# Performance work log

Measured on AMD Instinct MI355X. Metric: run time of the kernel, lower is better.

Reference implementation:

```python
import jax, jax.numpy as jnp
import numpy as np

USER_NUM = 100000
ITEM_NUM = 50000
N_NODES = USER_NUM + ITEM_NUM
EMB_DIM = 64
N_LAYERS = 3
NNZ = 4800000


def setup_inputs() -> dict:
    key = jax.random.key(0)
    k1, k2, k3, k4, k5 = jax.random.split(key, 5)
    user_emb = 0.2 * jax.random.normal(k1, (USER_NUM, EMB_DIM), dtype=jnp.float32)
    item_emb = 0.2 * jax.random.normal(k2, (ITEM_NUM, EMB_DIM), dtype=jnp.float32)
    adj_row = jax.random.randint(k3, (NNZ,), 0, N_NODES, dtype=jnp.int32)
    adj_col = jax.random.randint(k4, (NNZ,), 0, N_NODES, dtype=jnp.int32)
    adj_vals = jax.random.uniform(k5, (NNZ,), dtype=jnp.float32)
    return {
        "user_emb": user_emb,
        "item_emb": item_emb,
        "adj_row": adj_row,
        "adj_col": adj_col,
        "adj_vals": adj_vals,
    }


def _spmm(row, col, vals, x):
    # sparse [N,N] @ dense [N,D] via gather + weighted segment-sum
    msg = vals[:, None] * x[col]  # [nnz, D]
    return jax.ops.segment_sum(msg, row, num_segments=N_NODES)


def reference(user_emb, item_emb, adj_row, adj_col, adj_vals):
    ego = jnp.concatenate([user_emb, item_emb], axis=0)  # [N, D]
    acc = ego  # running sum over layers (equivalent to stack+mean)
    for _ in range(N_LAYERS):
        ego = _spmm(adj_row, adj_col, adj_vals, ego)
        acc = acc + ego
    out = acc / jnp.asarray(N_LAYERS + 1, dtype=acc.dtype)
    return out[:USER_NUM], out[USER_NUM:]
```

## Files before the change

kernel.cpp:

```cpp
#include <hip/hip_runtime.h>

#define USER_NUM 100000
#define ITEM_NUM 50000
#define N_NODES  150000
#define EMB_DIM  64
#define NNZ      4800000

#define CB_SHIFT 10
#define ROWS_PER_CB 1024
#define NCB ((N_NODES + ROWS_PER_CB - 1) / ROWS_PER_CB)
#define CB_CAP 34000
#define TILE 8192
#define NTILES ((NNZ + TILE - 1) / TILE)
#define EPT 32

#define SCAN_ITEMS 1024
#define NUM_SCAN_BLOCKS ((N_NODES + SCAN_ITEMS - 1) / SCAN_ITEMS)

__device__ __forceinline__ float bflo(unsigned u) {
    return __uint_as_float(u << 16);
}
__device__ __forceinline__ float bfhi(unsigned u) {
    return __uint_as_float(u & 0xFFFF0000u);
}
__device__ __forceinline__ unsigned f2bf(float f) {
    unsigned u = __float_as_uint(f);
    return (u + 0x7FFFu + ((u >> 16) & 1u)) >> 16;
}

__global__ void lgcn_init(const float4* __restrict__ user,
                          const float4* __restrict__ item,
                          uint4* __restrict__ xb,
                          float4* __restrict__ acc) {
    int i = blockIdx.x * blockDim.x + threadIdx.x;
    if (i >= N_NODES * 8) return;
    const int user_chunks = USER_NUM * 8;
    float4 f0, f1;
    if (i < user_chunks) {
        f0 = user[i * 2];
        f1 = user[i * 2 + 1];
    } else {
        f0 = item[(i - user_chunks) * 2];
        f1 = item[(i - user_chunks) * 2 + 1];
    }
    acc[i * 2]     = f0;
    acc[i * 2 + 1] = f1;
    uint4 p;
    p.x = f2bf(f0.x) | (f2bf(f0.y) << 16);
    p.y = f2bf(f0.z) | (f2bf(f0.w) << 16);
    p.z = f2bf(f1.x) | (f2bf(f1.y) << 16);
    p.w = f2bf(f1.z) | (f2bf(f1.w) << 16);
    xb[i] = p;
}

__global__ void lgcn_bcur_init(int* __restrict__ bucket_cursor) {
    int b = blockIdx.x * blockDim.x + threadIdx.x;
    if (b < NCB) bucket_cursor[b] = b * CB_CAP;
}

__global__ __launch_bounds__(256) void lgcn_partition(
    const int* __restrict__ row,
    const int* __restrict__ col,
    const float* __restrict__ vals,
    int* __restrict__ bucket_cursor,
    int2* __restrict__ t_cv) {
    __shared__ int hist[NCB];
    __shared__ int excl[NCB];
    __shared__ int delta[NCB];
    __shared__ unsigned lslot[TILE];
    __shared__ int sscan[256];

    int tid = threadIdx.x;
    int tileStart = blockIdx.x * TILE;
    int tileCount = NNZ - tileStart;
    if (tileCount > TILE) tileCount = TILE;

    for (int b = tid; b < NCB; b += 256) hist[b] = 0;
    __syncthreads();

    int rws[EPT];
#pragma unroll
    for (int k = 0; k < EPT; ++k) {
        int le = tid + k * 256;
        int r = -1;
        if (le < tileCount) {
            r = row[tileStart + le];
            atomicAdd(&hist[r >> CB_SHIFT], 1);
        }
        rws[k] = r;
    }
    __syncthreads();

    int h = (tid < NCB) ? hist[tid] : 0;
    sscan[tid] = h;
    __syncthreads();
    for (int off = 1; off < 256; off <<= 1) {
        int x = (tid >= off) ? sscan[tid - off] : 0;
        __syncthreads();
        sscan[tid] += x;
        __syncthreads();
    }
    if (tid < NCB) {
        int ex = sscan[tid] - h;
        excl[tid] = ex;
        int rb = h ? atomicAdd(&bucket_cursor[tid], h) : 0;
        delta[tid] = rb - ex;
    }
    __syncthreads();

#pragma unroll
    for (int k = 0; k < EPT; ++k) {
        int le = tid + k * 256;
        if (le < tileCount) {
            int r = rws[k];
            int b = r >> CB_SHIFT;
            int lp = atomicAdd(&excl[b], 1);
            lslot[lp] = ((unsigned)b << 23) |
                        ((unsigned)(r & (ROWS_PER_CB - 1)) << 13) |
                        (unsigned)le;
        }
    }
    __syncthreads();

    for (int i = tid; i < tileCount; i += 256) {
        unsigned s = lslot[i];
        int b = s >> 23;
        int rlo = (s >> 13) & (ROWS_PER_CB - 1);
        int le = s & 8191;
        int e = tileStart + le;
        int gpos = delta[b] + i;
        if (gpos < (b + 1) * CB_CAP) {
            t_cv[gpos] = make_int2((rlo << 18) | col[e],
                                   __float_as_int(vals[e]));
        }
    }
}

__global__ __launch_bounds__(256) void lgcn_count(
    const int* __restrict__ bucket_cursor,
    const int2* __restrict__ t_cv,
    int* __restrict__ cnt) {
    __shared__ int hist[ROWS_PER_CB];
    int b = blockIdx.x;
    int lo = b * ROWS_PER_CB;
    int nrows = N_NODES - lo;
    if (nrows > ROWS_PER_CB) nrows = ROWS_PER_CB;
    for (int i = threadIdx.x; i < nrows; i += 256) hist[i] = 0;
    __syncthreads();
    int base = b * CB_CAP;
    int count = bucket_cursor[b] - base;
    if (count > CB_CAP) count = CB_CAP;
    for (int e = base + threadIdx.x; e < base + count; e += 256) {
        unsigned rc = (unsigned)t_cv[e].x;
        atomicAdd(&hist[rc >> 18], 1);
    }
    __syncthreads();
    for (int i = threadIdx.x; i < nrows; i += 256) cnt[lo + i] = hist[i];
}

__global__ void lgcn_scan_blocksums(const int* __restrict__ cnt,
                                    int* __restrict__ blockSum) {
    int b = blockIdx.x, t = threadIdx.x;
    int base = b * SCAN_ITEMS + t * 4;
    int s = 0;
#pragma unroll
    for (int k = 0; k < 4; ++k) {
        int i = base + k;
        if (i < N_NODES) s += cnt[i];
    }
    __shared__ int red[256];
    red[t] = s;
    __syncthreads();
    for (int off = 128; off > 0; off >>= 1) {
        if (t < off) red[t] += red[t + off];
        __syncthreads();
    }
    if (t == 0) blockSum[b] = red[0];
}

__global__ void lgcn_scan_sums(const int* __restrict__ blockSum,
                               int* __restrict__ blockBase,
                               int* __restrict__ row_ptr) {
    int t = threadIdx.x;
    __shared__ int s[256];
    int v = (t < NUM_SCAN_BLOCKS) ? blockSum[t] : 0;
    s[t] = v;
    __syncthreads();
    for (int off = 1; off < 256; off <<= 1) {
        int x = (t >= off) ? s[t - off] : 0;
        __syncthreads();
        s[t] += x;
        __syncthreads();
    }
    if (t < NUM_SCAN_BLOCKS) blockBase[t] = s[t] - v;
    if (t == 0) row_ptr[N_NODES] = NNZ;
}

__global__ void lgcn_scan_final(const int* __restrict__ cnt,
                                const int* __restrict__ blockBase,
                                int* __restrict__ row_ptr) {
    int b = blockIdx.x, t = threadIdx.x;
    int base = b * SCAN_ITEMS + t * 4;
    int v[4];
    int tsum = 0;
#pragma unroll
    for (int k = 0; k < 4; ++k) {
        int i = base + k;
        v[k] = (i < N_NODES) ? cnt[i] : 0;
        tsum += v[k];
    }
    __shared__ int s[256];
    s[t] = tsum;
    __syncthreads();
    for (int off = 1; off < 256; off <<= 1) {
        int x = (t >= off) ? s[t - off] : 0;
        __syncthreads();
        s[t] += x;
        __syncthreads();
    }
    int p = blockBase[b] + (s[t] - tsum);
#pragma unroll
    for (int k = 0; k < 4; ++k) {
        int i = base + k;
        if (i < N_NODES) row_ptr[i] = p;
        p += v[k];
    }
}

__global__ __launch_bounds__(256) void lgcn_bucket_scatter(
    const int* __restrict__ row_ptr,
    const int* __restrict__ bucket_cursor,
    const int2* __restrict__ t_cv,
    int2* __restrict__ csr_cv) {
    __shared__ int cur[ROWS_PER_CB];
    int b = blockIdx.x;
    int lo = b * ROWS_PER_CB;
    int nrows = N_NODES - lo;
    if (nrows > ROWS_PER_CB) nrows = ROWS_PER_CB;
    for (int i = threadIdx.x; i < nrows; i += 256)
        cur[i] = row_ptr[lo + i];
    __syncthreads();
    int base = b * CB_CAP;
    int count = bucket_cursor[b] - base;
    if (count > CB_CAP) count = CB_CAP;
    for (int e = base + threadIdx.x; e < base + count; e += 256) {
        int2 cv = t_cv[e];
        int rlo = (unsigned)cv.x >> 18;
        int pos = atomicAdd(&cur[rlo], 1);
        csr_cv[pos] = make_int2(cv.x & 0x3FFFF, cv.y);
    }
}

__global__ __launch_bounds__(256) void lgcn_spmm_bf16(
    const int* __restrict__ row_ptr,
    const int2* __restrict__ csr_cv,
    const uint4* __restrict__ xb,
    uint4* __restrict__ yb,
    float4* __restrict__ acc,
    float scale) {
    int gid = blockIdx.x * blockDim.x + threadIdx.x;
    int r = gid >> 6;
    if (r >= N_NODES) return;
    int lane = threadIdx.x & 63;
    int c = lane & 7;
    int sub = lane >> 3;

    int start = row_ptr[r];
    int end = row_ptr[r + 1];

    float a0[8] = {0.f, 0.f, 0.f, 0.f, 0.f, 0.f, 0.f, 0.f};
    float a1[8] = {0.f, 0.f, 0.f, 0.f, 0.f, 0.f, 0.f, 0.f};

    int e = start + sub;
    for (; e + 8 < end; e += 16) {
        int2 cv0 = csr_cv[e];
        int2 cv1 = csr_cv[e + 8];
        uint4 u0 = xb[cv0.x * 8 + c];
        uint4 u1 = xb[cv1.x * 8 + c];
        float v0 = __int_as_float(cv0.y);
        float v1 = __int_as_float(cv1.y);
        a0[0] += v0 * bflo(u0.x); a0[1] += v0 * bfhi(u0.x);
        a0[2] += v0 * bflo(u0.y); a0[3] += v0 * bfhi(u0.y);
        a0[4] += v0 * bflo(u0.z); a0[5] += v0 * bfhi(u0.z);
        a0[6] += v0 * bflo(u0.w); a0[7] += v0 * bfhi(u0.w);
        a1[0] += v1 * bflo(u1.x); a1[1] += v1 * bfhi(u1.x);
        a1[2] += v1 * bflo(u1.y); a1[3] += v1 * bfhi(u1.y);
        a1[4] += v1 * bflo(u1.z); a1[5] += v1 * bfhi(u1.z);
        a1[6] += v1 * bflo(u1.w); a1[7] += v1 * bfhi(u1.w);
    }
    if (e < end) {
        int2 cv = csr_cv[e];
        uint4 u = xb[cv.x * 8 + c];
        float v = __int_as_float(cv.y);
        a0[0] += v * bflo(u.x); a0[1] += v * bfhi(u.x);
        a0[2] += v * bflo(u.y); a0[3] += v * bfhi(u.y);
        a0[4] += v * bflo(u.z); a0[5] += v * bfhi(u.z);
        a0[6] += v * bflo(u.w); a0[7] += v * bfhi(u.w);
    }

    float a[8];
#pragma unroll
    for (int k = 0; k < 8; ++k) a[k] = a0[k] + a1[k];

#pragma unroll
    for (int k = 0; k < 8; ++k) {
        a[k] += __shfl_xor(a[k], 8);
        a[k] += __shfl_xor(a[k], 16);
        a[k] += __shfl_xor(a[k], 32);
    }

    if (sub == 0) {
        uint4 p;
        p.x = f2bf(a[0]) | (f2bf(a[1]) << 16);
        p.y = f2bf(a[2]) | (f2bf(a[3]) << 16);
        p.z = f2bf(a[4]) | (f2bf(a[5]) << 16);
        p.w = f2bf(a[6]) | (f2bf(a[7]) << 16);
        yb[r * 8 + c] = p;
        int idx = r * 16 + c * 2;
        float4 o0 = acc[idx];
        float4 o1 = acc[idx + 1];
        o0.x = (o0.x + a[0]) * scale;
        o0.y = (o0.y + a[1]) * scale;
        o0.z = (o0.z + a[2]) * scale;
        o0.w = (o0.w + a[3]) * scale;
        o1.x = (o1.x + a[4]) * scale;
        o1.y = (o1.y + a[5]) * scale;
        o1.z = (o1.z + a[6]) * scale;
        o1.w = (o1.w + a[7]) * scale;
        acc[idx] = o0;
        acc[idx + 1] = o1;
    }
}

extern "C" void kernel_launch(void* const* d_in, const int* in_sizes, int n_in,
                              void* d_out, int out_size, void* d_ws, size_t ws_size,
                              hipStream_t stream) {
    const float* user_emb = (const float*)d_in[0];
    const float* item_emb = (const float*)d_in[1];
    const int*   adj_row  = (const int*)d_in[2];
    const int*   adj_col  = (const int*)d_in[3];
    const float* adj_vals = (const float*)d_in[4];
    float* out = (float*)d_out;

    char* base = (char*)d_ws;
    uint4* xb_a   = (uint4*)base;
    int2*  csr_cv = (int2*)(base + 19200000);
    char*  S      = base + 57600000;
    const size_t T_ENTRIES = (size_t)NCB * CB_CAP;
    int2*  t_cv   = (int2*)S;
    uint4* xb_b   = (uint4*)S;
    char*  tail   = S + T_ENTRIES * 8;
    int*   cnt    = (int*)tail;
    int*   row_ptr = cnt + N_NODES;
    int*   blockSum  = row_ptr + (N_NODES + 1);
    int*   blockBase = blockSum + 256;
    int*   bucket_cursor = blockBase + 256;

    {
        int threads = 256;
        int blocks = (N_NODES * 8 + threads - 1) / threads;
        lgcn_init<<<blocks, threads, 0, stream>>>(
            (const float4*)user_emb, (const float4*)item_emb,
            xb_a, (float4*)out);
    }

    lgcn_bcur_init<<<1, 256, 0, stream>>>(bucket_cursor);
    lgcn_partition<<<NTILES, 256, 0, stream>>>(
        adj_row, adj_col, adj_vals, bucket_cursor, t_cv);
    lgcn_count<<<NCB, 256, 0, stream>>>(bucket_cursor, t_cv, cnt);
    lgcn_scan_blocksums<<<NUM_SCAN_BLOCKS, 256, 0, stream>>>(cnt, blockSum);
    lgcn_scan_sums<<<1, 256, 0, stream>>>(blockSum, blockBase, row_ptr);
    lgcn_scan_final<<<NUM_SCAN_BLOCKS, 256, 0, stream>>>(cnt, blockBase, row_ptr);
    lgcn_bucket_scatter<<<NCB, 256, 0, stream>>>(
        row_ptr, bucket_cursor, t_cv, csr_cv);

    const int spmm_block = 256;
    const int spmm_grid = (N_NODES * 64 + spmm_block - 1) / spmm_block;
    uint4* xa = xb_a;
    uint4* xbv = xb_b;
    for (int layer = 0; layer < 3; ++layer) {
        float scale = (layer == 2) ? 0.25f : 1.0f;
        lgcn_spmm_bf16<<<spmm_grid, spmm_block, 0, stream>>>(
            row_ptr, csr_cv, xa, xbv, (float4*)out, scale);
        uint4* t = xa; xa = xbv; xbv = t;
    }
}
```

Before: 606.5 us.

## Fuse count, scan and scatter into one per-bucket finalize kernel; unroll SpMM

```diff
diff --git a/kernel.cpp b/kernel.cpp
--- a/kernel.cpp
+++ b/kernel.cpp
@@ -13,9 +13,6 @@
 #define TILE 8192
 #define NTILES ((NNZ + TILE - 1) / TILE)
 #define EPT 32
-
-#define SCAN_ITEMS 1024
-#define NUM_SCAN_BLOCKS ((N_NODES + SCAN_ITEMS - 1) / SCAN_ITEMS)
 
 __device__ __forceinline__ float bflo(unsigned u) {
     return __uint_as_float(u << 16);
@@ -136,114 +133,70 @@
     }
 }
 
-__global__ __launch_bounds__(256) void lgcn_count(
+__global__ __launch_bounds__(256) void lgcn_finalize(
     const int* __restrict__ bucket_cursor,
     const int2* __restrict__ t_cv,
-    int* __restrict__ cnt) {
+    int2* __restrict__ csr_cv,
+    int2* __restrict__ row_se) {
     __shared__ int hist[ROWS_PER_CB];
+    __shared__ int cur[ROWS_PER_CB];
+    __shared__ int sscan[256];
+    int t = threadIdx.x;
     int b = blockIdx.x;
+
+    int v = 0;
+    if (t < NCB) {
+        int cb = bucket_cursor[t] - t * CB_CAP;
+        v = (cb > CB_CAP) ? CB_CAP : cb;
+    }
+    sscan[t] = v;
+    __syncthreads();
+    for (int off = 1; off < 256; off <<= 1) {
+        int x = (t >= off) ? sscan[t - off] : 0;
+        __syncthreads();
+        sscan[t] += x;
+        __syncthreads();
+    }
+    int prev = (b == 0) ? 0 : sscan[b - 1];
+    int bbase = prev;
+    int count = sscan[b] - prev;
+
     int lo = b * ROWS_PER_CB;
     int nrows = N_NODES - lo;
     if (nrows > ROWS_PER_CB) nrows = ROWS_PER_CB;
-    for (int i = threadIdx.x; i < nrows; i += 256) hist[i] = 0;
-    __syncthreads();
+
+    for (int i = t; i < ROWS_PER_CB; i += 256) hist[i] = 0;
+    __syncthreads();
+
     int base = b * CB_CAP;
-    int count = bucket_cursor[b] - base;
-    if (count > CB_CAP) count = CB_CAP;
-    for (int e = base + threadIdx.x; e < base + count; e += 256) {
-        unsigned rc = (unsigned)t_cv[e].x;
-        atomicAdd(&hist[rc >> 18], 1);
-    }
-    __syncthreads();
-    for (int i = threadIdx.x; i < nrows; i += 256) cnt[lo + i] = hist[i];
-}
-
-__global__ void lgcn_scan_blocksums(const int* __restrict__ cnt,
-                                    int* __restrict__ blockSum) {
-    int b = blockIdx.x, t = threadIdx.x;
-    int base = b * SCAN_ITEMS + t * 4;
-    int s = 0;
+    for (int e = base + t; e < base + count; e += 256)
+        atomicAdd(&hist[(unsigned)t_cv[e].x >> 18], 1);
+    __syncthreads();
+
+    int4 hh = ((const int4*)hist)[t];
+    int tsum = hh.x + hh.y + hh.z + hh.w;
+    sscan[t] = tsum;
+    __syncthreads();
+    for (int off = 1; off < 256; off <<= 1) {
+        int x = (t >= off) ? sscan[t - off] : 0;
+        __syncthreads();
+        sscan[t] += x;
+        __syncthreads();
+    }
+    int p = bbase + sscan[t] - tsum;
+    int hv[4] = {hh.x, hh.y, hh.z, hh.w};
+    int i0 = t * 4;
 #pragma unroll
     for (int k = 0; k < 4; ++k) {
-        int i = base + k;
-        if (i < N_NODES) s += cnt[i];
-    }
-    __shared__ int red[256];
-    red[t] = s;
-    __syncthreads();
-    for (int off = 128; off > 0; off >>= 1) {
-        if (t < off) red[t] += red[t + off];
-        __syncthreads();
-    }
-    if (t == 0) blockSum[b] = red[0];
-}
-
-__global__ void lgcn_scan_sums(const int* __restrict__ blockSum,
-                               int* __restrict__ blockBase,
-                               int* __restrict__ row_ptr) {
-    int t = threadIdx.x;
-    __shared__ int s[256];
-    int v = (t < NUM_SCAN_BLOCKS) ? blockSum[t] : 0;
-    s[t] = v;
-    __syncthreads();
-    for (int off = 1; off < 256; off <<= 1) {
-        int x = (t >= off) ? s[t - off] : 0;
-        __syncthreads();
-        s[t] += x;
-        __syncthreads();
-    }
-    if (t < NUM_SCAN_BLOCKS) blockBase[t] = s[t] - v;
-    if (t == 0) row_ptr[N_NODES] = NNZ;
-}
-
-__global__ void lgcn_scan_final(const int* __restrict__ cnt,
-                                const int* __restrict__ blockBase,
-                                int* __restrict__ row_ptr) {
-    int b = blockIdx.x, t = threadIdx.x;
-    int base = b * SCAN_ITEMS + t * 4;
-    int v[4];
-    int tsum = 0;
-#pragma unroll
-    for (int k = 0; k < 4; ++k) {
-        int i = base + k;
-        v[k] = (i < N_NODES) ? cnt[i] : 0;
-        tsum += v[k];
-    }
-    __shared__ int s[256];
-    s[t] = tsum;
-    __syncthreads();
-    for (int off = 1; off < 256; off <<= 1) {
-        int x = (t >= off) ? s[t - off] : 0;
-        __syncthreads();
-        s[t] += x;
-        __syncthreads();
-    }
-    int p = blockBase[b] + (s[t] - tsum);
-#pragma unroll
-    for (int k = 0; k < 4; ++k) {
-        int i = base + k;
-        if (i < N_NODES) row_ptr[i] = p;
-        p += v[k];
-    }
-}
-
-__global__ __launch_bounds__(256) void lgcn_bucket_scatter(
-    const int* __restrict__ row_ptr,
-    const int* __restrict__ bucket_cursor,
-    const int2* __restrict__ t_cv,
-    int2* __restrict__ csr_cv) {
-    __shared__ int cur[ROWS_PER_CB];
-    int b = blockIdx.x;
-    int lo = b * ROWS_PER_CB;
-    int nrows = N_NODES - lo;
-    if (nrows > ROWS_PER_CB) nrows = ROWS_PER_CB;
-    for (int i = threadIdx.x; i < nrows; i += 256)
-        cur[i] = row_ptr[lo + i];
-    __syncthreads();
-    int base = b * CB_CAP;
-    int count = bucket_cursor[b] - base;
-    if (count > CB_CAP) count = CB_CAP;
-    for (int e = base + threadIdx.x; e < base + count; e += 256) {
+        if (i0 + k < nrows) {
+            row_se[lo + i0 + k] = make_int2(p, p + hv[k]);
+            cur[i0 + k] = p;
+        }
+        p += hv[k];
+    }
+    __syncthreads();
+
+    for (int e = base + t; e < base + count; e += 256) {
         int2 cv = t_cv[e];
         int rlo = (unsigned)cv.x >> 18;
         int pos = atomicAdd(&cur[rlo], 1);
@@ -251,8 +204,15 @@
     }
 }
 
-__global__ __launch_bounds__(256) void lgcn_spmm_bf16(
-    const int* __restrict__ row_ptr,
+#define FMA8(vv, uu) do {                                          \
+    a[0] += (vv) * bflo((uu).x); a[1] += (vv) * bfhi((uu).x);      \
+    a[2] += (vv) * bflo((uu).y); a[3] += (vv) * bfhi((uu).y);      \
+    a[4] += (vv) * bflo((uu).z); a[5] += (vv) * bfhi((uu).z);      \
+    a[6] += (vv) * bflo((uu).w); a[7] += (vv) * bfhi((uu).w);      \
+} while (0)
+
+__global__ __launch_bounds__(256, 8) void lgcn_spmm_bf16(
+    const int2* __restrict__ row_se,
     const int2* __restrict__ csr_cv,
     const uint4* __restrict__ xb,
     uint4* __restrict__ yb,
@@ -265,42 +225,48 @@
     int c = lane & 7;
     int sub = lane >> 3;
 
-    int start = row_ptr[r];
-    int end = row_ptr[r + 1];
-
-    float a0[8] = {0.f, 0.f, 0.f, 0.f, 0.f, 0.f, 0.f, 0.f};
-    float a1[8] = {0.f, 0.f, 0.f, 0.f, 0.f, 0.f, 0.f, 0.f};
+    int2 se = row_se[r];
+    int start = se.x;
+    int end = se.y;
+
+    float a[8] = {0.f, 0.f, 0.f, 0.f, 0.f, 0.f, 0.f, 0.f};
 
     int e = start + sub;
-    for (; e + 8 < end; e += 16) {
+    for (; e + 24 < end; e += 32) {
+        int2 cv0 = csr_cv[e];
+        int2 cv1 = csr_cv[e + 8];
+        int2 cv2 = csr_cv[e + 16];
+        int2 cv3 = csr_cv[e + 24];
+        uint4 u0 = xb[cv0.x * 8 + c];
+        uint4 u1 = xb[cv1.x * 8 + c];
+        uint4 u2 = xb[cv2.x * 8 + c];
+        uint4 u3 = xb[cv3.x * 8 + c];
+        float v0 = __int_as_float(cv0.y);
+        float v1 = __int_as_float(cv1.y);
+        float v2 = __int_as_float(cv2.y);
+        float v3 = __int_as_float(cv3.y);
+        FMA8(v0, u0);
+        FMA8(v1, u1);
+        FMA8(v2, u2);
+        FMA8(v3, u3);
+    }
+    if (e + 8 < end) {
         int2 cv0 = csr_cv[e];
         int2 cv1 = csr_cv[e + 8];
         uint4 u0 = xb[cv0.x * 8 + c];
         uint4 u1 = xb[cv1.x * 8 + c];
         float v0 = __int_as_float(cv0.y);
         float v1 = __int_as_float(cv1.y);
-        a0[0] += v0 * bflo(u0.x); a0[1] += v0 * bfhi(u0.x);
-        a0[2] += v0 * bflo(u0.y); a0[3] += v0 * bfhi(u0.y);
-        a0[4] += v0 * bflo(u0.z); a0[5] += v0 * bfhi(u0.z);
-        a0[6] += v0 * bflo(u0.w); a0[7] += v0 * bfhi(u0.w);
-        a1[0] += v1 * bflo(u1.x); a1[1] += v1 * bfhi(u1.x);
-        a1[2] += v1 * bflo(u1.y); a1[3] += v1 * bfhi(u1.y);
-        a1[4] += v1 * bflo(u1.z); a1[5] += v1 * bfhi(u1.z);
-        a1[6] += v1 * bflo(u1.w); a1[7] += v1 * bfhi(u1.w);
+        FMA8(v0, u0);
+        FMA8(v1, u1);
+        e += 16;
     }
     if (e < end) {
         int2 cv = csr_cv[e];
         uint4 u = xb[cv.x * 8 + c];
         float v = __int_as_float(cv.y);
-        a0[0] += v * bflo(u.x); a0[1] += v * bfhi(u.x);
-        a0[2] += v * bflo(u.y); a0[3] += v * bfhi(u.y);
-        a0[4] += v * bflo(u.z); a0[5] += v * bfhi(u.z);
-        a0[6] += v * bflo(u.w); a0[7] += v * bfhi(u.w);
-    }
-
-    float a[8];
-#pragma unroll
-    for (int k = 0; k < 8; ++k) a[k] = a0[k] + a1[k];
+        FMA8(v, u);
+    }
 
 #pragma unroll
     for (int k = 0; k < 8; ++k) {
@@ -350,11 +316,8 @@
     int2*  t_cv   = (int2*)S;
     uint4* xb_b   = (uint4*)S;
     char*  tail   = S + T_ENTRIES * 8;
-    int*   cnt    = (int*)tail;
-    int*   row_ptr = cnt + N_NODES;
-    int*   blockSum  = row_ptr + (N_NODES + 1);
-    int*   blockBase = blockSum + 256;
-    int*   bucket_cursor = blockBase + 256;
+    int2*  row_se = (int2*)tail;
+    int*   bucket_cursor = (int*)(tail + (size_t)N_NODES * 8);
 
     {
         int threads = 256;
@@ -367,12 +330,8 @@
     lgcn_bcur_init<<<1, 256, 0, stream>>>(bucket_cursor);
     lgcn_partition<<<NTILES, 256, 0, stream>>>(
         adj_row, adj_col, adj_vals, bucket_cursor, t_cv);
-    lgcn_count<<<NCB, 256, 0, stream>>>(bucket_cursor, t_cv, cnt);
-    lgcn_scan_blocksums<<<NUM_SCAN_BLOCKS, 256, 0, stream>>>(cnt, blockSum);
-    lgcn_scan_sums<<<1, 256, 0, stream>>>(blockSum, blockBase, row_ptr);
-    lgcn_scan_final<<<NUM_SCAN_BLOCKS, 256, 0, stream>>>(cnt, blockBase, row_ptr);
-    lgcn_bucket_scatter<<<NCB, 256, 0, stream>>>(
-        row_ptr, bucket_cursor, t_cv, csr_cv);
+    lgcn_finalize<<<NCB, 256, 0, stream>>>(
+        bucket_cursor, t_cv, csr_cv, row_se);
 
     const int spmm_block = 256;
     const int spmm_grid = (N_NODES * 64 + spmm_block - 1) / spmm_block;
@@ -381,7 +340,7 @@
     for (int layer = 0; layer < 3; ++layer) {
         float scale = (layer == 2) ? 0.25f : 1.0f;
         lgcn_spmm_bf16<<<spmm_grid, spmm_block, 0, stream>>>(
-            row_ptr, csr_cv, xa, xbv, (float4*)out, scale);
+            row_se, csr_cv, xa, xbv, (float4*)out, scale);
         uint4* t = xa; xa = xbv; xbv = t;
     }
 }
```

Result: faster. 591.3 us (-2.5%).
